# Kernel optimization log

Hardware: AMD Instinct MI355X
Metric: run time of the kernel (lower is better)

## Reference

```python
import jax, jax.numpy as jnp
import numpy as np

D_IN = 2048
D_OUT = 2048
NUM_HEADS = 16
NUM_GROUPS = 4
HEAD_DIM = D_OUT // NUM_HEADS          # 128
HEADS_PER_GROUP = NUM_HEADS // NUM_GROUPS  # 4


def setup_inputs() -> dict:
    key = jax.random.key(0)
    ks = jax.random.split(key, 6)
    b, s = 2, 2048
    x = jax.random.normal(ks[0], (b, s, D_IN), dtype=jnp.float32)
    # Store weights as [in, out] so y = x @ W (equivalent to torch Linear x @ W.T)
    sc_q = 1.0 / np.sqrt(D_IN)
    Wq = jax.random.uniform(ks[1], (D_IN, D_OUT), jnp.float32, -sc_q, sc_q)
    Wk = jax.random.uniform(ks[2], (D_IN, NUM_GROUPS * HEAD_DIM), jnp.float32, -sc_q, sc_q)
    Wv = jax.random.uniform(ks[3], (D_IN, NUM_GROUPS * HEAD_DIM), jnp.float32, -sc_q, sc_q)
    sc_o = 1.0 / np.sqrt(D_OUT)
    Wo = jax.random.uniform(ks[4], (D_OUT, D_OUT), jnp.float32, -sc_o, sc_o)
    bo = jax.random.uniform(ks[5], (D_OUT,), jnp.float32, -sc_o, sc_o)
    return {"x": x, "Wq": Wq, "Wk": Wk, "Wv": Wv, "Wo": Wo, "bo": bo}


def reference(x, Wq, Wk, Wv, Wo, bo):
    b, s, _ = x.shape
    g, hpg, hd = NUM_GROUPS, HEADS_PER_GROUP, HEAD_DIM
    # Projections; keep grouped layout instead of repeat_interleave (same math)
    q = (x @ Wq).reshape(b, s, g, hpg, hd)   # query heads ordered group-major,
                                             # matching repeat_interleave of K/V
    k = (x @ Wk).reshape(b, s, g, hd)
    v = (x @ Wv).reshape(b, s, g, hd)
    # scores: [b, g, hpg, q_len, k_len]
    scores = jnp.einsum('bqghd,bkgd->bghqk', q, k)
    causal = jnp.triu(jnp.ones((s, s), dtype=bool), k=1)  # True above diagonal
    scores = jnp.where(causal, -jnp.inf, scores)
    scale = 1.0 / jnp.sqrt(jnp.asarray(hd, dtype=scores.dtype))
    attn = jax.nn.softmax(scores * scale, axis=-1)
    ctx = jnp.einsum('bghqk,bkgd->bqghd', attn, v).reshape(b, s, D_OUT)
    return ctx @ Wo + bo
```

## Files before the change

kernel.cpp:

```cpp
#include <hip/hip_runtime.h>

typedef short v8s __attribute__((ext_vector_type(8)));
typedef float v4f __attribute__((ext_vector_type(4)));

__device__ __forceinline__ short f2bf(float f) {
  union { float f; unsigned u; } v; v.f = f;
  unsigned r = v.u + 0x7FFFu + ((v.u >> 16) & 1u);
  return (short)(r >> 16);
}

__device__ __forceinline__ void gll16(const short* g, short* l) {
  __builtin_amdgcn_global_load_lds(
      (const __attribute__((address_space(1))) void*)g,
      (__attribute__((address_space(3))) void*)l, 16, 0, 0);
}

__global__ void cast_and_transpose(const float* __restrict__ x, short* __restrict__ xb,
                                   const float* __restrict__ Wq, const float* __restrict__ Wk,
                                   const float* __restrict__ Wv, const float* __restrict__ Wo,
                                   short* __restrict__ Wqkvt, short* __restrict__ Wot) {
  const int tid = threadIdx.x;
  int bid = blockIdx.x;
  if (bid < 8192) {
    int i = bid * 256 + tid;
    float4 v = ((const float4*)x)[i];
    short4 o;
    o.x = f2bf(v.x); o.y = f2bf(v.y); o.z = f2bf(v.z); o.w = f2bf(v.w);
    ((short4*)xb)[i] = o;
    return;
  }
  __shared__ float tile[32][33];
  bid -= 8192;
  const int tx = tid & 31, ty = tid >> 5;
  int bx = bid % 160;
  const int byy = bid / 160;
  const float* src; short* dst; int C, cb; float fac = 1.0f;
  if (bx < 64)      { src = Wq; dst = Wqkvt;                        C = 2048; cb = bx;
                      fac = 0.08838834764831845f * 1.4426950408889634f; }
  else if (bx < 80) { src = Wk; dst = Wqkvt + (size_t)2048 * 2048;  C = 512;  cb = bx - 64; }
  else if (bx < 96) { src = Wv; dst = Wqkvt + (size_t)2560 * 2048;  C = 512;  cb = bx - 80; }
  else              { src = Wo; dst = Wot;                          C = 2048; cb = bx - 96; }
  const int c0 = cb * 32, r0 = byy * 32;
#pragma unroll
  for (int i = 0; i < 4; ++i)
    tile[ty + 8 * i][tx] = src[(size_t)(r0 + ty + 8 * i) * C + c0 + tx];
  __syncthreads();
#pragma unroll
  for (int i = 0; i < 4; ++i)
    dst[(size_t)(c0 + ty + 8 * i) * 2048 + r0 + tx] = f2bf(tile[tx][ty + 8 * i] * fac);
}

__global__ void transpose_v_perm(const short* __restrict__ qkv, short* __restrict__ out) {
  __shared__ short tile[32][33];
  const int tx = threadIdx.x, ty = threadIdx.y;
  const int c0 = blockIdx.x * 32, r0 = blockIdx.y * 32;
  const int z = blockIdx.z;
#pragma unroll
  for (int i = 0; i < 4; ++i)
    tile[ty + 8 * i][tx] = qkv[(size_t)(z * 2048 + r0 + ty + 8 * i) * 3072 + 2560 + c0 + tx];
  __syncthreads();
#pragma unroll
  for (int i = 0; i < 4; ++i) {
    int k = r0 + tx;
    int pk = (k & ~31) | ((((k >> 2) & 3) * 2 + ((k >> 4) & 1)) * 4) | (k & 3);
    out[(size_t)z * 512 * 2048 + (size_t)(c0 + ty + 8 * i) * 2048 + pk] = tile[tx][ty + 8 * i];
  }
}

template <int BF16_OUT>
__global__ __launch_bounds__(256, 3) void gemm_bt2p(const short* __restrict__ A,
                                                    const short* __restrict__ Bt,
                                                    void* __restrict__ Cout,
                                                    const float* __restrict__ bias,
                                                    int N, int K, int nbx, int cpx) {
  __shared__ __align__(16) short sm[2 * 8192];
  const int tid = threadIdx.x;
  const int w = tid >> 6, lane = tid & 63, quad = lane >> 4, l16 = lane & 15;
  const int wm = (w >> 1) * 64, wn = (w & 1) * 64;
  const int bid = blockIdx.x;
  const int swz = (bid & 7) * cpx + (bid >> 3);
  const int n0 = (swz % nbx) * 128, m0 = (swz / nbx) * 128;
  const int NT = K >> 5;

  const int srow = lane >> 2;
  const int sc = ((lane & 3) ^ ((lane >> 2) & 3) ^ ((lane >> 4) & 3)) * 8;
  const short* Ag = A + (size_t)(m0 + w * 16 + srow) * K + sc;
  const short* Bg = Bt + (size_t)(n0 + w * 16 + srow) * K + sc;
  short* Ad = sm + w * 512 + lane * 8;
  short* Bd = sm + 4096 + w * 512 + lane * 8;
  const size_t rjump = (size_t)64 * K;

  auto stage = [&](int t, int bf_) {
    const int k = t << 5;
    short* ad = Ad + bf_ * 8192;
    short* bd = Bd + bf_ * 8192;
    gll16(Ag + k, ad);
    gll16(Ag + k + rjump, ad + 2048);
    gll16(Bg + k, bd);
    gll16(Bg + k + rjump, bd + 2048);
  };

  const int rsc = (quad ^ (l16 & 3) ^ ((l16 >> 2) & 3)) * 8;
  const short* aBase = sm + (wm + l16) * 32 + rsc;
  const short* bBase = sm + 4096 + (wn + l16) * 32 + rsc;

  v4f acc[4][4] = {};

  stage(0, 0);
  __syncthreads();

  for (int t = 0; t < NT; ++t) {
    if (t + 1 < NT) stage(t + 1, (t + 1) & 1);
    const int bo_ = (t & 1) * 8192;
    v8s af[4], bf[4];
#pragma unroll
    for (int i = 0; i < 4; ++i) af[i] = *(const v8s*)(aBase + bo_ + i * 512);
#pragma unroll
    for (int i = 0; i < 4; ++i) bf[i] = *(const v8s*)(bBase + bo_ + i * 512);
    __builtin_amdgcn_s_setprio(1);
#pragma unroll
    for (int mi = 0; mi < 4; ++mi)
#pragma unroll
      for (int ni = 0; ni < 4; ++ni)
        acc[mi][ni] = __builtin_amdgcn_mfma_f32_16x16x32_bf16(af[mi], bf[ni], acc[mi][ni], 0, 0, 0);
    __builtin_amdgcn_s_setprio(0);
    if (t + 1 < NT) __syncthreads();
  }

#pragma unroll
  for (int mi = 0; mi < 4; ++mi) {
#pragma unroll
    for (int ni = 0; ni < 4; ++ni) {
      const int col = n0 + wn + ni * 16 + l16;
#pragma unroll
      for (int r = 0; r < 4; ++r) {
        const int row = m0 + wm + mi * 16 + quad * 4 + r;
        if (BF16_OUT) {
          ((short*)Cout)[(size_t)row * N + col] = f2bf(acc[mi][ni][r]);
        } else {
          ((float*)Cout)[(size_t)row * N + col] = acc[mi][ni][r] + bias[col];
        }
      }
    }
  }
}

__global__ __launch_bounds__(512, 4) void flash_attn7(const short* __restrict__ QKV,
                                                      const short* __restrict__ Vtb,
                                                      short* __restrict__ ctx) {
  __shared__ __align__(16) short smem[32768];
  const int tid = threadIdx.x;
  const int w = tid >> 6, lane = tid & 63, quad = lane >> 4, l16 = lane & 15;
  const int wq = w >> 1, wk = w & 1;
  const int bh = blockIdx.y;
  const int b = bh >> 4, h = bh & 15, g = h >> 2;
  v8s ones;
#pragma unroll
  for (int i = 0; i < 8; ++i) ones[i] = (short)0x3F80;

  const int krl = lane >> 4, kcl = lane & 15;
  const int vrl = lane >> 3, vcl = lane & 7;
  const short* Kg0 = QKV + (size_t)(b * 2048 + w * 8 + krl) * 3072 + 2048 + g * 128;
  const short* Vg0 = Vtb + (size_t)(b * 512 + g * 128 + w * 16 + vrl) * 2048 + (vcl ^ (vrl & 7)) * 8;
  short* kd = smem + (w * 8) * 128 + lane * 8;
  short* vd = smem + 8192 + (w * 16) * 64 + lane * 8;

  auto stage = [&](int key0, int bs) {
    const short* kg = Kg0 + (size_t)key0 * 3072;
    const short* vg = Vg0 + key0;
#pragma unroll
    for (int ii = 0; ii < 2; ++ii) {
      const int rl = (w & 1) * 8 + ii * 4 + krl;
      gll16(kg + (size_t)(ii * 4) * 3072 + (kcl ^ rl) * 8, kd + bs * 16384 + ii * 512);
      gll16(vg + (size_t)(ii * 8) * 2048, vd + bs * 16384 + ii * 512);
    }
  };

  float* red = (float*)smem;

#pragma unroll 1
  for (int half = 0; half < 2; ++half) {
    const int qt = half ? (31 - blockIdx.x) : blockIdx.x;
    const int q0 = qt * 64;
    const int qb = q0 + wq * 16;

    v8s aq[4];
    {
      const short* Qp = QKV + (size_t)(b * 2048 + qb + l16) * 3072 + h * 128 + quad * 8;
#pragma unroll
      for (int kk = 0; kk < 4; ++kk) aq[kk] = *(const v8s*)(Qp + kk * 32);
    }
    v4f o[8] = {};
    v4f ol = {};

    __syncthreads();
    stage(0, 0);
    const int nk = qt + 1;
#pragma unroll 1
    for (int kt = 0; kt < nk; ++kt) {
      const int key0 = kt << 6;
      __syncthreads();
      if (kt + 1 < nk) stage((kt + 1) << 6, (kt + 1) & 1);
      const short* Ks = smem + (kt & 1) * 16384;
      const short* Vs = Ks + 8192;
      const int kb = key0 + wk * 32;
      if (kb > qb + 15) continue;
      v4f sf[2] = {};
      __builtin_amdgcn_s_setprio(1);
#pragma unroll
      for (int kfl = 0; kfl < 2; ++kfl)
#pragma unroll
        for (int kk = 0; kk < 4; ++kk) {
          v8s kfr = *(const v8s*)&Ks[((wk * 2 + kfl) * 16 + l16) * 128 + (((kk * 4 + quad) ^ l16) * 8)];
          sf[kfl] = __builtin_amdgcn_mfma_f32_16x16x32_bf16(kfr, aq[kk], sf[kfl], 0, 0, 0);
        }
      __builtin_amdgcn_s_setprio(0);
      const bool diag = (kb + 31 > qb);
      const int qg = qb + l16;
      union { v8s v; unsigned u[4]; } pu;
#pragma unroll
      for (int kfl = 0; kfl < 2; ++kfl) {
        float e[4];
#pragma unroll
        for (int r = 0; r < 4; ++r) {
          float s = sf[kfl][r];
          if (diag && (kb + kfl * 16 + quad * 4 + r > qg)) s = -1e30f;
          e[r] = exp2f(s);
        }
        asm("v_cvt_pk_bf16_f32 %0, %1, %2" : "=v"(pu.u[kfl * 2 + 0]) : "v"(e[0]), "v"(e[1]));
        asm("v_cvt_pk_bf16_f32 %0, %1, %2" : "=v"(pu.u[kfl * 2 + 1]) : "v"(e[2]), "v"(e[3]));
      }
      const v8s pa = pu.v;
      __builtin_amdgcn_s_setprio(1);
#pragma unroll
      for (int nf = 0; nf < 8; ++nf) {
        v8s vf = *(const v8s*)&Vs[(nf * 16 + l16) * 64 + (((wk * 4 + quad) ^ (l16 & 7)) * 8)];
        o[nf] = __builtin_amdgcn_mfma_f32_16x16x32_bf16(pa, vf, o[nf], 0, 0, 0);
      }
      ol = __builtin_amdgcn_mfma_f32_16x16x32_bf16(pa, ones, ol, 0, 0, 0);
      __builtin_amdgcn_s_setprio(0);
    }
    __syncthreads();

    if (wk == 1)
      *(v4f*)&red[wq * 256 + l16 * 16 + quad * 4] = ol;
    __syncthreads();
    if (wk == 0)
      ol += *(const v4f*)&red[wq * 256 + l16 * 16 + quad * 4];
    __syncthreads();
    if (wk == 1) {
#pragma unroll
      for (int nf = 0; nf < 8; ++nf)
        *(v4f*)&red[(wq * 8 + nf) * 256 + l16 * 16 + quad * 4] = o[nf];
    }
    __syncthreads();
    if (wk == 0) {
      float inv[4];
#pragma unroll
      for (int r = 0; r < 4; ++r) inv[r] = 1.0f / ol[r];
#pragma unroll
      for (int nf = 0; nf < 8; ++nf) {
        v4f osum = o[nf] + *(const v4f*)&red[(wq * 8 + nf) * 256 + l16 * 16 + quad * 4];
#pragma unroll
        for (int r = 0; r < 4; ++r) {
          const int row = qb + quad * 4 + r;
          ctx[(size_t)(b * 2048 + row) * 2048 + h * 128 + nf * 16 + l16] = f2bf(osum[r] * inv[r]);
        }
      }
    }
  }
}

extern "C" void kernel_launch(void* const* d_in, const int* in_sizes, int n_in,
                              void* d_out, int out_size, void* d_ws, size_t ws_size,
                              hipStream_t stream) {
  const float* x = (const float*)d_in[0];
  const float* Wq = (const float*)d_in[1];
  const float* Wk = (const float*)d_in[2];
  const float* Wv = (const float*)d_in[3];
  const float* Wo = (const float*)d_in[4];
  const float* bo = (const float*)d_in[5];
  float* out = (float*)d_out;
  char* ws = (char*)d_ws;

  short* xb    = (short*)(ws);
  short* ctx   = (short*)(ws);
  short* Wqkvt = (short*)(ws + 16777216);
  short* Wot   = (short*)(ws + 29360128);
  short* QKV   = (short*)(ws + 37748736);
  short* Vtb   = (short*)(ws + 62914560);

  cast_and_transpose<<<18432, 256, 0, stream>>>(x, xb, Wq, Wk, Wv, Wo, Wqkvt, Wot);

  gemm_bt2p<1><<<768, 256, 0, stream>>>(xb, Wqkvt, (void*)QKV, nullptr, 3072, 2048, 24, 96);

  transpose_v_perm<<<dim3(16, 64, 2), dim3(32, 8), 0, stream>>>(QKV, Vtb);

  flash_attn7<<<dim3(16, 32), 512, 0, stream>>>(QKV, Vtb, ctx);

  gemm_bt2p<0><<<512, 256, 0, stream>>>(ctx, Wot, (void*)out, bo, 2048, 2048, 16, 64);
}
```

Before: 279.6 us.

## Load GEMM B fragments directly from global into registers, bypassing LDS

The GEMM kernel stops staging the B tile through shared memory. Each wave now loads its own B fragments straight from global memory into registers, double-buffered with a loop unrolled by two, while A is still staged in LDS. This halves LDS use and LDS traffic, which could allow more resident blocks. In exchange, B rows are loaded redundantly by the two waves that share the same columns, global loads are less coalesced, register pressure rises, and the loop assumes the K-tile count is even.

```diff
diff --git a/kernel.cpp b/kernel.cpp
--- a/kernel.cpp
+++ b/kernel.cpp
@@ -73,7 +73,7 @@
                                                     void* __restrict__ Cout,
                                                     const float* __restrict__ bias,
                                                     int N, int K, int nbx, int cpx) {
-  __shared__ __align__(16) short sm[2 * 8192];
+  __shared__ __align__(16) short sm[2 * 4096];
   const int tid = threadIdx.x;
   const int w = tid >> 6, lane = tid & 63, quad = lane >> 4, l16 = lane & 15;
   const int wm = (w >> 1) * 64, wn = (w & 1) * 64;
@@ -85,46 +85,66 @@
   const int srow = lane >> 2;
   const int sc = ((lane & 3) ^ ((lane >> 2) & 3) ^ ((lane >> 4) & 3)) * 8;
   const short* Ag = A + (size_t)(m0 + w * 16 + srow) * K + sc;
-  const short* Bg = Bt + (size_t)(n0 + w * 16 + srow) * K + sc;
   short* Ad = sm + w * 512 + lane * 8;
-  short* Bd = sm + 4096 + w * 512 + lane * 8;
   const size_t rjump = (size_t)64 * K;
 
-  auto stage = [&](int t, int bf_) {
+  auto stageA = [&](int t, int bf_) {
     const int k = t << 5;
-    short* ad = Ad + bf_ * 8192;
-    short* bd = Bd + bf_ * 8192;
+    short* ad = Ad + bf_ * 4096;
     gll16(Ag + k, ad);
     gll16(Ag + k + rjump, ad + 2048);
-    gll16(Bg + k, bd);
-    gll16(Bg + k + rjump, bd + 2048);
   };
 
   const int rsc = (quad ^ (l16 & 3) ^ ((l16 >> 2) & 3)) * 8;
   const short* aBase = sm + (wm + l16) * 32 + rsc;
-  const short* bBase = sm + 4096 + (wn + l16) * 32 + rsc;
+
+  const short* Bgf = Bt + (size_t)(n0 + wn + l16) * K + quad * 8;
+  auto loadB = [&](v8s* dst, int t) {
+    const short* p = Bgf + (t << 5);
+#pragma unroll
+    for (int i = 0; i < 4; ++i) dst[i] = *(const v8s*)(p + (size_t)(i * 16) * K);
+  };
 
   v4f acc[4][4] = {};
-
-  stage(0, 0);
+  v8s b0[4], b1[4];
+
+  stageA(0, 0);
+  loadB(b0, 0);
   __syncthreads();
 
-  for (int t = 0; t < NT; ++t) {
-    if (t + 1 < NT) stage(t + 1, (t + 1) & 1);
-    const int bo_ = (t & 1) * 8192;
-    v8s af[4], bf[4];
-#pragma unroll
-    for (int i = 0; i < 4; ++i) af[i] = *(const v8s*)(aBase + bo_ + i * 512);
-#pragma unroll
-    for (int i = 0; i < 4; ++i) bf[i] = *(const v8s*)(bBase + bo_ + i * 512);
-    __builtin_amdgcn_s_setprio(1);
-#pragma unroll
-    for (int mi = 0; mi < 4; ++mi)
-#pragma unroll
-      for (int ni = 0; ni < 4; ++ni)
-        acc[mi][ni] = __builtin_amdgcn_mfma_f32_16x16x32_bf16(af[mi], bf[ni], acc[mi][ni], 0, 0, 0);
-    __builtin_amdgcn_s_setprio(0);
-    if (t + 1 < NT) __syncthreads();
+  for (int t = 0; t < NT; t += 2) {
+    {
+      stageA(t + 1, 1);
+      loadB(b1, t + 1);
+      v8s af[4];
+#pragma unroll
+      for (int i = 0; i < 4; ++i) af[i] = *(const v8s*)(aBase + i * 512);
+      __builtin_amdgcn_s_setprio(1);
+#pragma unroll
+      for (int mi = 0; mi < 4; ++mi)
+#pragma unroll
+        for (int ni = 0; ni < 4; ++ni)
+          acc[mi][ni] = __builtin_amdgcn_mfma_f32_16x16x32_bf16(af[mi], b0[ni], acc[mi][ni], 0, 0, 0);
+      __builtin_amdgcn_s_setprio(0);
+      __syncthreads();
+    }
+    {
+      if (t + 2 < NT) {
+        stageA(t + 2, 0);
+        loadB(b0, t + 2);
+      }
+      v8s af[4];
+#pragma unroll
+      for (int i = 0; i < 4; ++i) af[i] = *(const v8s*)(aBase + 4096 + i * 512);
+      __builtin_amdgcn_s_setprio(1);
+#pragma unroll
+      for (int mi = 0; mi < 4; ++mi)
+#pragma unroll
+        for (int ni = 0; ni < 4; ++ni)
+          acc[mi][ni] = __builtin_amdgcn_mfma_f32_16x16x32_bf16(af[mi], b1[ni], acc[mi][ni], 0, 0, 0);
+      __builtin_amdgcn_s_setprio(0);
+      if (t + 2 < NT) __syncthreads();
+    }
   }
 
 #pragma unroll
```

Result: slower. 387.8 us (+38.7%).
